# Performance work log

Hardware: AMD Instinct MI355X
Metric: run time of the kernel (lower is better)

The kernel has to match this reference:

```python
import jax, jax.numpy as jnp
import numpy as np
import math

B, S, D, H, NB = 32, 512, 512, 8, 2
DK = D // H
DF = 4 * D
EPS = 1e-8


def layer_norm(x, gamma, beta):
    # Matches torch: unbiased std (ddof=1), divide by (std + eps)
    mean = jnp.mean(x, axis=-1, keepdims=True)
    std = jnp.sqrt(jnp.var(x, axis=-1, keepdims=True, ddof=1))
    return gamma * (x - mean) / (std + EPS) + beta


def block(x, wq, bq, wk, bk, wv, bv, wr, br, ga, ba, wc1, bc1, wc2, bc2, gf, bf):
    # --- attention with ReLU-gated Q/K/V ---
    Q = jax.nn.relu(x @ wq.T + bq)  # [B,S,D]
    K = jax.nn.relu(x @ wk.T + bk)
    V = jax.nn.relu(x @ wv.T + bv)
    # chunk along last dim -> heads; head-major stacking is equivalent to this reshape
    Qh = Q.reshape(B, S, H, DK)
    Kh = K.reshape(B, S, H, DK)
    Vh = V.reshape(B, S, H, DK)
    scores = jnp.einsum('bqhd,bkhd->bhqk', Qh, Kh) / math.sqrt(DK)
    w = jax.nn.softmax(scores, axis=-1)
    out = jnp.einsum('bhqk,bkhd->bqhd', w, Vh).reshape(B, S, D)
    out = out + jax.nn.relu(x @ wr.T + br)
    out = layer_norm(out, ga, ba)
    # --- conv1d (kernel=1) feed-forward ---
    h = jax.nn.relu(out @ wc1.T + bc1)  # [B,S,4D]
    y = h @ wc2.T + bc2                 # [B,S,D]
    y = layer_norm(y + out, gf, bf)
    return y


def setup_inputs() -> dict:
    key = jax.random.key(0)
    ks = jax.random.split(key, 8)
    std = 0.01
    inp = {
        'x': jax.random.normal(ks[0], (B, S, D), jnp.float32),
        'wq': jax.random.normal(ks[1], (NB, D, D), jnp.float32) * std,
        'bq': jnp.zeros((NB, D), jnp.float32),
        'wk': jax.random.normal(ks[2], (NB, D, D), jnp.float32) * std,
        'bk': jnp.zeros((NB, D), jnp.float32),
        'wv': jax.random.normal(ks[3], (NB, D, D), jnp.float32) * std,
        'bv': jnp.zeros((NB, D), jnp.float32),
        'wr': jax.random.normal(ks[4], (NB, D, D), jnp.float32) * std,
        'br': jnp.zeros((NB, D), jnp.float32),
        'g_attn': jnp.ones((NB, D), jnp.float32),
        'b_attn': jnp.zeros((NB, D), jnp.float32),
        'wc1': jax.random.normal(ks[5], (NB, DF, D), jnp.float32) * (1.0 / math.sqrt(D)),
        'bc1': jnp.zeros((NB, DF), jnp.float32),
        'wc2': jax.random.normal(ks[6], (NB, D, DF), jnp.float32) * (1.0 / math.sqrt(DF)),
        'bc2': jnp.zeros((NB, D), jnp.float32),
        'g_ffn': jnp.ones((NB, D), jnp.float32),
        'b_ffn': jnp.zeros((NB, D), jnp.float32),
    }
    return inp


def reference(x, wq, bq, wk, bk, wv, bv, wr, br, g_attn, b_attn,
              wc1, bc1, wc2, bc2, g_ffn, b_ffn):
    enc = x
    for i in range(NB):
        enc = block(enc, wq[i], bq[i], wk[i], bk[i], wv[i], bv[i], wr[i], br[i],
                    g_attn[i], b_attn[i], wc1[i], bc1[i], wc2[i], bc2[i],
                    g_ffn[i], b_ffn[i])
    return enc
```

## Files before the change

### kernel.cpp

```cpp
#include <hip/hip_runtime.h>

typedef unsigned short u16;
typedef __bf16 bf16x8 __attribute__((ext_vector_type(8)));
typedef float f32x4 __attribute__((ext_vector_type(4)));
typedef unsigned short ushort8 __attribute__((ext_vector_type(8)));

__device__ __forceinline__ void gload_lds16(const void* g, void* l) {
  __builtin_amdgcn_global_load_lds(
      (const __attribute__((address_space(1))) void*)g,
      (__attribute__((address_space(3))) void*)l, 16, 0, 0);
}

__device__ __forceinline__ u16 f2bf(float f) {
  unsigned int u = __builtin_bit_cast(unsigned int, f);
  u = (u + 0x7fffu + ((u >> 16) & 1u)) >> 16;
  return (u16)u;
}
__device__ __forceinline__ u16 f2bf_trunc(float f) {
  return (u16)(__builtin_bit_cast(unsigned int, f) >> 16);
}
__device__ __forceinline__ float bf2f(u16 u) {
  unsigned int v = (unsigned int)u << 16;
  return __builtin_bit_cast(float, v);
}

__global__ void castk(const float* __restrict__ in, u16* __restrict__ out, int n,
                      float scale) {
  size_t i = ((size_t)blockIdx.x * 256 + threadIdx.x) * 8;
  if (i >= (size_t)n) return;
  const float4* p = (const float4*)(in + i);
  float4 a = p[0], b = p[1];
  ushort8 o;
  o[0] = f2bf(a.x * scale); o[1] = f2bf(a.y * scale);
  o[2] = f2bf(a.z * scale); o[3] = f2bf(a.w * scale);
  o[4] = f2bf(b.x * scale); o[5] = f2bf(b.y * scale);
  o[6] = f2bf(b.z * scale); o[7] = f2bf(b.w * scale);
  *(ushort8*)(out + i) = o;
}

__global__ void biasg(const float* __restrict__ b0, const float* __restrict__ b1,
                      const float* __restrict__ b2, const float* __restrict__ b3,
                      float* __restrict__ out) {
  int idx = blockIdx.x * 256 + threadIdx.x;
  int i = idx >> 11, j = (idx >> 9) & 3, c = idx & 511;
  const float* src = (j == 0) ? b0 : (j == 1) ? b1 : (j == 2) ? b2 : b3;
  float v = src[i * 512 + c];
  out[idx] = (j == 0) ? v * 0.125f : v;
}

template<int BN, int RELU, int WVT>
__global__ __launch_bounds__(512, 2)
void gemm8(const u16* __restrict__ A, const u16* __restrict__ W,
           const float* __restrict__ bias, u16* __restrict__ C,
           u16* __restrict__ VT, int M, int N, int K)
{
  constexpr int WN = (BN == 256) ? 4 : 2;
  constexpr int WM = 8 / WN;
  constexpr int RM = 256 / WM;
  constexpr int MF = RM / 16;
  constexpr int ASZ = 16384;
  constexpr int BSZ = BN * 64;
  constexpr int ALOADS = 2;
  constexpr int BLOADS = BN / 128;
  constexpr int VC = ALOADS + BLOADS;

  __shared__ u16 lds[(ASZ + BSZ) * 2];
  char* Abase = (char*)lds;
  char* Bbase = (char*)lds + ASZ * 4;

  const int tid = threadIdx.x;
  const int w = tid >> 6, l = tid & 63;
  const int nbn = N / BN;
  const int p = blockIdx.x;
  const int x = p & 7, i0 = p >> 3;
  const int bm = x * 8 + i0 / nbn;
  const int bn = i0 % nbn;
  const int wn = w & (WN - 1);
  const int wm = w / WN;
  const int NK = K >> 5;

  const int srow = l >> 2;
  const int scol = ((l & 3) ^ ((l >> 3) & 3)) << 3;
  const u16* aS[ALOADS];
  const u16* bS[BLOADS];
#pragma unroll
  for (int u = 0; u < ALOADS; ++u)
    aS[u] = A + (size_t)(bm * 256 + (u * 8 + w) * 16 + srow) * K + scol;
#pragma unroll
  for (int u = 0; u < BLOADS; ++u)
    bS[u] = W + (size_t)(bn * BN + (u * 8 + w) * 16 + srow) * K + scol;

  auto stage = [&](int t) {
    const int bsel = t & 3;
#pragma unroll
    for (int u = 0; u < ALOADS; ++u)
      gload_lds16(aS[u] + t * 32, Abase + bsel * ASZ + (u * 8 + w) * 1024);
#pragma unroll
    for (int u = 0; u < BLOADS; ++u)
      gload_lds16(bS[u] + t * 32, Bbase + bsel * BSZ + (u * 8 + w) * 1024);
  };

  f32x4 acc[MF][4] = {};

  stage(0); stage(1); stage(2);

  for (int t = 0; t < NK; ++t) {
    const int rem = NK - 1 - t;
    if (rem >= 2)      asm volatile("s_waitcnt vmcnt(%0)" :: "i"(2 * VC) : "memory");
    else if (rem == 1) asm volatile("s_waitcnt vmcnt(%0)" :: "i"(VC) : "memory");
    else               asm volatile("s_waitcnt vmcnt(0)" ::: "memory");
    __builtin_amdgcn_s_barrier();
    __builtin_amdgcn_sched_barrier(0);
    if (t + 3 < NK) stage(t + 3);

    const char* Ab = Abase + (t & 3) * ASZ;
    const char* Bb = Bbase + (t & 3) * BSZ;
    bf16x8 af[MF], bfv[4];
#pragma unroll
    for (int mi = 0; mi < MF; ++mi) {
      int row = wm * RM + mi * 16 + (l & 15);
      af[mi] = *(const bf16x8*)(Ab + row * 64 + (((l >> 4) ^ ((row >> 1) & 3)) << 4));
    }
#pragma unroll
    for (int ni = 0; ni < 4; ++ni) {
      int row = wn * 64 + ni * 16 + (l & 15);
      bfv[ni] = *(const bf16x8*)(Bb + row * 64 + (((l >> 4) ^ ((row >> 1) & 3)) << 4));
    }
    __builtin_amdgcn_s_setprio(1);
#pragma unroll
    for (int mi = 0; mi < MF; ++mi)
#pragma unroll
      for (int ni = 0; ni < 4; ++ni)
        acc[mi][ni] = __builtin_amdgcn_mfma_f32_16x16x32_bf16(af[mi], bfv[ni], acc[mi][ni], 0, 0, 0);
    __builtin_amdgcn_s_setprio(0);
  }

  __syncthreads();
  char* Ct = (char*)lds;
  const int rowL = wm * RM + ((l >> 4) << 2);
  const int colL = wn * 64 + (l & 15);
  const bool dovt = WVT && (bn == 4 || bn == 5);
  float bv[4];
#pragma unroll
  for (int ni = 0; ni < 4; ++ni) bv[ni] = bias[bn * BN + colL + ni * 16];

  if (!dovt) {
#pragma unroll
    for (int mi = 0; mi < MF; ++mi)
#pragma unroll
      for (int ni = 0; ni < 4; ++ni)
#pragma unroll
        for (int r = 0; r < 4; ++r) {
          float v = acc[mi][ni][r] + bv[ni];
          if (RELU) v = fmaxf(v, 0.f);
          int m = rowL + mi * 16 + r, n = colL + ni * 16;
          *(u16*)(Ct + m * (BN * 2) + ((n * 2) ^ ((m & 7) << 4))) = f2bf(v);
        }
    __syncthreads();
    constexpr int TPR = (BN * 2) / 16;
    constexpr int RPP = 512 / TPR;
#pragma unroll
    for (int pass = 0; pass < 256 / RPP; ++pass) {
      int row = pass * RPP + tid / TPR;
      int c16 = tid % TPR;
      bf16x8 vv = *(const bf16x8*)(Ct + row * (BN * 2) + ((c16 * 16) ^ ((row & 7) << 4)));
      *(bf16x8*)(&C[(size_t)(bm * 256 + row) * N + bn * BN + c16 * 8]) = vv;
    }
  } else {
#pragma unroll
    for (int mi = 0; mi < MF; ++mi)
#pragma unroll
      for (int ni = 0; ni < 4; ++ni)
#pragma unroll
        for (int r = 0; r < 4; ++r) {
          float v = acc[mi][ni][r] + bv[ni];
          if (RELU) v = fmaxf(v, 0.f);
          int m = rowL + mi * 16 + r, d = colL + ni * 16;
          *(u16*)(Ct + d * 512 + ((m * 2) ^ ((d & 7) << 4))) = f2bf(v);
        }
    __syncthreads();
    const int batch = bm >> 1;
#pragma unroll
    for (int pass = 0; pass < 16; ++pass) {
      int dL = pass * 16 + (tid >> 5);
      int m16 = tid & 31;
      bf16x8 vv = *(const bf16x8*)(Ct + dL * 512 + ((m16 * 16) ^ ((dL & 7) << 4)));
      int head = (bn - 4) * 4 + (dL >> 6);
      int vtr = (batch * 8 + head) * 64 + (dL & 63);
      *(bf16x8*)(&VT[(size_t)vtr * 512 + (bm & 1) * 256 + m16 * 8]) = vv;
    }
  }
}

__global__ __launch_bounds__(256, 2)
void attn_kernel(const u16* __restrict__ qkvr, const u16* __restrict__ VT,
                 u16* __restrict__ F)
{
  const int D4 = 2048;
  __shared__ u16 Qs[128 * 64];
  __shared__ u16 Ks[2][64 * 64];
  __shared__ u16 Vs[2][64 * 64];
  __shared__ u16 Ps[128 * 64];

  const int tid = threadIdx.x, w = tid >> 6, l = tid & 63;
  const int bh = blockIdx.x & 255, qt = blockIdx.x >> 8;
  const int b = bh >> 3, h = bh & 7;
  const int lr = l >> 3, lc = ((l & 7) ^ lr) << 3;
  const int l15 = l & 15, lh = l >> 4;

  const u16* qG = qkvr + (size_t)(b * 512 + qt * 128) * D4 + h * 64 + lc;
#pragma unroll
  for (int i = 0; i < 4; ++i) {
    int c = w * 4 + i;
    gload_lds16(qG + (size_t)(c * 8 + lr) * D4, &Qs[c * 512]);
  }

  const u16* kG = qkvr + (size_t)(b * 512) * D4 + 512 + h * 64 + lc;
  const u16* vG = VT + (size_t)(bh * 64) * 512 + lc;

  auto stageKV = [&](int kt) {
    const int bsel = kt & 1;
#pragma unroll
    for (int i = 0; i < 2; ++i) {
      int c = w * 2 + i;
      gload_lds16(kG + (size_t)(kt * 64 + c * 8 + lr) * D4, &Ks[bsel][c * 512]);
      gload_lds16(vG + (size_t)(c * 8 + lr) * 512 + kt * 64, &Vs[bsel][c * 512]);
    }
  };
  stageKV(0);

  f32x4 o_acc[2][4] = {};
  float psum[2][4] = {};

  for (int kt = 0; kt < 8; ++kt) {
    __syncthreads();
    if (kt < 7) stageKV(kt + 1);
    const char* Kb = (const char*)Ks[kt & 1];
    const char* Vb = (const char*)Vs[kt & 1];

    f32x4 sacc[2][4] = {};
#pragma unroll
    for (int kk = 0; kk < 2; ++kk) {
      bf16x8 qa[2];
#pragma unroll
      for (int qq = 0; qq < 2; ++qq) {
        int qrow = w * 32 + qq * 16 + l15;
        qa[qq] = *(const bf16x8*)((const char*)Qs + qrow * 128 +
                  ((kk * 64 + (lh << 4)) ^ ((qrow & 7) << 4)));
      }
#pragma unroll
      for (int ni = 0; ni < 4; ++ni) {
        int krow = ni * 16 + l15;
        bf16x8 kb = *(const bf16x8*)(Kb + krow * 128 +
                    ((kk * 64 + (lh << 4)) ^ ((krow & 7) << 4)));
#pragma unroll
        for (int qq = 0; qq < 2; ++qq)
          sacc[qq][ni] = __builtin_amdgcn_mfma_f32_16x16x32_bf16(qa[qq], kb, sacc[qq][ni], 0, 0, 0);
      }
    }

#pragma unroll
    for (int qq = 0; qq < 2; ++qq)
#pragma unroll
      for (int r = 0; r < 4; ++r) {
        float p0 = __expf(sacc[qq][0][r]);
        float p1 = __expf(sacc[qq][1][r]);
        float p2 = __expf(sacc[qq][2][r]);
        float p3 = __expf(sacc[qq][3][r]);
        psum[qq][r] += (p0 + p1) + (p2 + p3);
        int q = w * 32 + qq * 16 + (lh << 2) + r;
        int sw = (q & 7) << 4;
        int col = l15 * 2;
        char* pb = (char*)Ps + q * 128;
        *(u16*)(pb + ((0  + col) ^ sw)) = f2bf_trunc(p0);
        *(u16*)(pb + ((32 + col) ^ sw)) = f2bf_trunc(p1);
        *(u16*)(pb + ((64 + col) ^ sw)) = f2bf_trunc(p2);
        *(u16*)(pb + ((96 + col) ^ sw)) = f2bf_trunc(p3);
      }

#pragma unroll
    for (int kk = 0; kk < 2; ++kk) {
      bf16x8 pa[2];
#pragma unroll
      for (int qq = 0; qq < 2; ++qq) {
        int qrow = w * 32 + qq * 16 + l15;
        pa[qq] = *(const bf16x8*)((const char*)Ps + qrow * 128 +
                  ((kk * 64 + (lh << 4)) ^ ((qrow & 7) << 4)));
      }
#pragma unroll
      for (int ni = 0; ni < 4; ++ni) {
        int d = ni * 16 + l15;
        bf16x8 vb = *(const bf16x8*)(Vb + d * 128 +
                    ((kk * 64 + (lh << 4)) ^ ((d & 7) << 4)));
#pragma unroll
        for (int qq = 0; qq < 2; ++qq)
          o_acc[qq][ni] = __builtin_amdgcn_mfma_f32_16x16x32_bf16(pa[qq], vb, o_acc[qq][ni], 0, 0, 0);
      }
    }
  }

  float lsum[2][4];
#pragma unroll
  for (int qq = 0; qq < 2; ++qq)
#pragma unroll
    for (int r = 0; r < 4; ++r) {
      float t = psum[qq][r];
#pragma unroll
      for (int m = 1; m < 16; m <<= 1) t += __shfl_xor(t, m);
      lsum[qq][r] = 1.f / t;
    }

#pragma unroll
  for (int qq = 0; qq < 2; ++qq)
#pragma unroll
    for (int ni = 0; ni < 4; ++ni) {
      int d = ni * 16 + l15;
#pragma unroll
      for (int r = 0; r < 4; ++r) {
        float v = o_acc[qq][ni][r] * lsum[qq][r];
        int q = w * 32 + qq * 16 + (lh << 2) + r;
        *(u16*)((char*)Ps + q * 128 + ((d * 2) ^ ((q & 7) << 4))) = f2bf(v);
      }
    }
  __syncthreads();
  const u16* Rbase = qkvr + (size_t)(b * 512 + qt * 128) * D4 + 1536 + h * 64;
  u16* Fbase = F + (size_t)(b * 512 + qt * 128) * 512 + h * 64;
#pragma unroll
  for (int pass = 0; pass < 4; ++pass) {
    int row = pass * 32 + (tid >> 3), c8 = tid & 7;
    ushort8 lv = *(const ushort8*)((char*)Ps + row * 128 + ((c8 * 16) ^ ((row & 7) << 4)));
    ushort8 rv = *(const ushort8*)(Rbase + (size_t)row * D4 + c8 * 8);
    ushort8 o;
#pragma unroll
    for (int j = 0; j < 8; ++j) o[j] = f2bf(bf2f(lv[j]) + bf2f(rv[j]));
    *(ushort8*)(Fbase + (size_t)row * 512 + c8 * 8) = o;
  }
}

template<int HAS_RES, int OUT_F32>
__global__ __launch_bounds__(256)
void ln_bf(const u16* __restrict__ in, const u16* __restrict__ res,
           const float* __restrict__ gamma, const float* __restrict__ beta,
           u16* __restrict__ outb, float* __restrict__ outf)
{
  const int l = threadIdx.x & 63;
  const size_t row = (size_t)blockIdx.x * 4 + (threadIdx.x >> 6);
  ushort8 iv = *(const ushort8*)(in + row * 512 + l * 8);
  float x[8];
#pragma unroll
  for (int j = 0; j < 8; ++j) x[j] = bf2f(iv[j]);
  if (HAS_RES) {
    ushort8 rv = *(const ushort8*)(res + row * 512 + l * 8);
#pragma unroll
    for (int j = 0; j < 8; ++j) x[j] += bf2f(rv[j]);
  }
  float s = 0.f, ss = 0.f;
#pragma unroll
  for (int j = 0; j < 8; ++j) { s += x[j]; ss += x[j] * x[j]; }
#pragma unroll
  for (int m = 1; m < 64; m <<= 1) { s += __shfl_xor(s, m); ss += __shfl_xor(ss, m); }
  float mean = s * (1.f / 512.f);
  float var = fmaxf((ss - 512.f * mean * mean) * (1.f / 511.f), 0.f);
  float inv = 1.f / (sqrtf(var) + 1e-8f);
  const float4* g4 = (const float4*)gamma;
  const float4* b4 = (const float4*)beta;
  float4 g0 = g4[l * 2], g1 = g4[l * 2 + 1];
  float4 b0 = b4[l * 2], b1 = b4[l * 2 + 1];
  float gg[8] = {g0.x, g0.y, g0.z, g0.w, g1.x, g1.y, g1.z, g1.w};
  float bb[8] = {b0.x, b0.y, b0.z, b0.w, b1.x, b1.y, b1.z, b1.w};
  float y[8];
#pragma unroll
  for (int j = 0; j < 8; ++j) y[j] = gg[j] * (x[j] - mean) * inv + bb[j];
  ushort8 o;
#pragma unroll
  for (int j = 0; j < 8; ++j) o[j] = f2bf(y[j]);
  *(ushort8*)(outb + row * 512 + l * 8) = o;
  if (OUT_F32) {
    float4* o4 = (float4*)(outf + row * 512);
    o4[l * 2]     = make_float4(y[0], y[1], y[2], y[3]);
    o4[l * 2 + 1] = make_float4(y[4], y[5], y[6], y[7]);
  }
}

extern "C" void kernel_launch(void* const* d_in, const int* in_sizes, int n_in,
                              void* d_out, int out_size, void* d_ws, size_t ws_size,
                              hipStream_t stream)
{
  const int B = 32, S = 512, D = 512, NB = 2, DF = 2048;
  const int M = B * S;

  const float* x   = (const float*)d_in[0];
  const float* wsrc[4] = {(const float*)d_in[1], (const float*)d_in[3],
                          (const float*)d_in[5], (const float*)d_in[7]};
  const float* ga  = (const float*)d_in[9];
  const float* ba  = (const float*)d_in[10];
  const float* wc1 = (const float*)d_in[11];
  const float* bc1 = (const float*)d_in[12];
  const float* wc2 = (const float*)d_in[13];
  const float* bc2 = (const float*)d_in[14];
  const float* gf  = (const float*)d_in[15];
  const float* bfp = (const float*)d_in[16];

  char* ws = (char*)d_ws;
  u16*   curb = (u16*)(ws + 0);
  u16*   qkvr = (u16*)(ws + 16777216);
  u16*   F    = (u16*)(ws + 83886080);
  u16*   Hg   = (u16*)(ws + 100663296);
  u16*   VT   = (u16*)(ws + 117440512);
  u16*   w4b  = (u16*)(ws + 134217728);
  u16*   wc1b = (u16*)(ws + 138412032);
  u16*   wc2b = (u16*)(ws + 142606336);
  float* b4   = (float*)(ws + 146800640);
  u16*   Ih   = qkvr;
  u16*   Y    = F;

  castk<<<M * D / 2048, 256, 0, stream>>>(x, curb, M * D, 1.0f);
  for (int i = 0; i < NB; ++i)
    for (int j = 0; j < 4; ++j)
      castk<<<128, 256, 0, stream>>>(wsrc[j] + (size_t)i * 262144,
                                     w4b + (size_t)i * 1048576 + j * 262144, 262144,
                                     (j == 0) ? 0.125f : 1.0f);
  biasg<<<16, 256, 0, stream>>>((const float*)d_in[2], (const float*)d_in[4],
                                (const float*)d_in[6], (const float*)d_in[8], b4);
  castk<<<NB * DF * D / 2048, 256, 0, stream>>>(wc1, wc1b, NB * DF * D, 1.0f);
  castk<<<NB * DF * D / 2048, 256, 0, stream>>>(wc2, wc2b, NB * DF * D, 1.0f);

  for (int i = 0; i < NB; ++i) {
    const size_t wfo = (size_t)i * DF * D;
    gemm8<256, 1, 1><<<512, 512, 0, stream>>>(curb, w4b + (size_t)i * 1048576,
                                              b4 + i * 2048, qkvr, VT, M, 2048, 512);
    attn_kernel<<<4 * 256, 256, 0, stream>>>(qkvr, VT, F);
    ln_bf<0, 0><<<M / 4, 256, 0, stream>>>(F, nullptr, ga + i * D, ba + i * D, Hg, nullptr);
    gemm8<256, 1, 0><<<512, 512, 0, stream>>>(Hg, wc1b + wfo, bc1 + i * DF,
                                              Ih, nullptr, M, 2048, 512);
    gemm8<128, 0, 0><<<256, 512, 0, stream>>>(Ih, wc2b + wfo, bc2 + i * D,
                                              Y, nullptr, M, 512, 2048);
    if (i == NB - 1)
      ln_bf<1, 1><<<M / 4, 256, 0, stream>>>(Y, Hg, gf + i * D, bfp + i * D,
                                             curb, (float*)d_out);
    else
      ln_bf<1, 0><<<M / 4, 256, 0, stream>>>(Y, Hg, gf + i * D, bfp + i * D,
                                             curb, nullptr);
  }
}
```

Before: 395.0 us.

## Restructure bf16 GEMM into 8-wave ping-pong pipeline with 64-wide K tiles

Replaces the GEMM main loop's 4-deep ring of 32-wide K stages with double-buffered 64-wide K tiles split into M and N halves. Each iteration runs four MFMA quadrants separated by barriers, and loads for the next tile are issued between them. Every wave now covers a 128-row M slice, and the layout switches to a 128-byte-row LDS swizzle. The goal is better overlap of global-to-LDS loads with MFMA work and fewer barriers per unit of K. In exchange it uses more accumulator and fragment registers plus extra intra-iteration barriers, which could lower occupancy under the 2-blocks-per-CU launch bound.

```diff
diff --git a/kernel.cpp b/kernel.cpp
--- a/kernel.cpp
+++ b/kernel.cpp
@@ -50,105 +50,113 @@
 
 template<int BN, int RELU, int WVT>
 __global__ __launch_bounds__(512, 2)
-void gemm8(const u16* __restrict__ A, const u16* __restrict__ W,
-           const float* __restrict__ bias, u16* __restrict__ C,
-           u16* __restrict__ VT, int M, int N, int K)
+void gemm256(const u16* __restrict__ A, const u16* __restrict__ W,
+             const float* __restrict__ bias, u16* __restrict__ C,
+             u16* __restrict__ VT, int M, int N, int K)
 {
-  constexpr int WN = (BN == 256) ? 4 : 2;
-  constexpr int WM = 8 / WN;
-  constexpr int RM = 256 / WM;
-  constexpr int MF = RM / 16;
-  constexpr int ASZ = 16384;
-  constexpr int BSZ = BN * 64;
-  constexpr int ALOADS = 2;
-  constexpr int BLOADS = BN / 128;
-  constexpr int VC = ALOADS + BLOADS;
-
-  __shared__ u16 lds[(ASZ + BSZ) * 2];
-  char* Abase = (char*)lds;
-  char* Bbase = (char*)lds + ASZ * 4;
-
-  const int tid = threadIdx.x;
-  const int w = tid >> 6, l = tid & 63;
+  constexpr int CN   = BN / 4;
+  constexpr int NF   = CN / 32;
+  constexpr int NTOT = CN / 16;
+  constexpr int ATSZ = 256 * 128;
+  constexpr int BTSZ = BN * 128;
+  constexpr int BLH  = BN / 128;
+
+  __shared__ char lds[2 * (ATSZ + BTSZ)];
+  char* ABase = lds;
+  char* BBase = lds + 2 * ATSZ;
+
+  const int tid = threadIdx.x, w = tid >> 6, l = tid & 63;
+  const int l15 = l & 15, lh = l >> 4;
   const int nbn = N / BN;
   const int p = blockIdx.x;
-  const int x = p & 7, i0 = p >> 3;
-  const int bm = x * 8 + i0 / nbn;
-  const int bn = i0 % nbn;
-  const int wn = w & (WN - 1);
-  const int wm = w / WN;
-  const int NK = K >> 5;
-
-  const int srow = l >> 2;
-  const int scol = ((l & 3) ^ ((l >> 3) & 3)) << 3;
-  const u16* aS[ALOADS];
-  const u16* bS[BLOADS];
-#pragma unroll
-  for (int u = 0; u < ALOADS; ++u)
-    aS[u] = A + (size_t)(bm * 256 + (u * 8 + w) * 16 + srow) * K + scol;
-#pragma unroll
-  for (int u = 0; u < BLOADS; ++u)
-    bS[u] = W + (size_t)(bn * BN + (u * 8 + w) * 16 + srow) * K + scol;
-
-  auto stage = [&](int t) {
-    const int bsel = t & 3;
-#pragma unroll
-    for (int u = 0; u < ALOADS; ++u)
-      gload_lds16(aS[u] + t * 32, Abase + bsel * ASZ + (u * 8 + w) * 1024);
-#pragma unroll
-    for (int u = 0; u < BLOADS; ++u)
-      gload_lds16(bS[u] + t * 32, Bbase + bsel * BSZ + (u * 8 + w) * 1024);
-  };
-
-  f32x4 acc[MF][4] = {};
-
-  stage(0); stage(1); stage(2);
-
-  for (int t = 0; t < NK; ++t) {
-    const int rem = NK - 1 - t;
-    if (rem >= 2)      asm volatile("s_waitcnt vmcnt(%0)" :: "i"(2 * VC) : "memory");
-    else if (rem == 1) asm volatile("s_waitcnt vmcnt(%0)" :: "i"(VC) : "memory");
-    else               asm volatile("s_waitcnt vmcnt(0)" ::: "memory");
+  const int bm = (p & 7) * 8 + (p >> 3) / nbn;
+  const int bn = (p >> 3) % nbn;
+  const int wm = w >> 2, wn = w & 3;
+  const int NT = K >> 6;
+
+  const int srow = l >> 3;
+  const int scol = ((l & 7) ^ srow) << 3;
+  const u16* aG = A + (size_t)(bm * 256 + srow) * K + scol;
+  const u16* bG = W + (size_t)(bn * BN + srow) * K + scol;
+
+#define STAGE_A(T, H)                                                          \
+  { _Pragma("unroll") for (int i = 0; i < 2; ++i)                              \
+      gload_lds16(aG + (size_t)((H) * 128 + (w * 2 + i) * 8) * K + (T) * 64,   \
+                  ABase + ((T) & 1) * ATSZ + (H) * 16384 + (w * 2 + i) * 1024); }
+#define STAGE_B(T, H)                                                          \
+  { _Pragma("unroll") for (int i = 0; i < BLH; ++i)                            \
+      gload_lds16(bG + (size_t)((H) * (BN / 2) + (w * BLH + i) * 8) * K + (T) * 64, \
+                  BBase + ((T) & 1) * BTSZ + (H) * (BTSZ / 2) + (w * BLH + i) * 1024); }
+#define READ_A(MH)                                                             \
+  { _Pragma("unroll") for (int kk = 0; kk < 2; ++kk)                           \
+    _Pragma("unroll") for (int mf = 0; mf < 4; ++mf) {                         \
+      int row = wm * 128 + (MH) * 64 + mf * 16 + l15;                          \
+      a[kk][mf] = *(const bf16x8*)(Ab + row * 128 +                            \
+                   ((kk * 64 + lh * 16) ^ ((l15 & 7) << 4)));                  \
+    } }
+#define READ_B(NH)                                                             \
+  { _Pragma("unroll") for (int kk = 0; kk < 2; ++kk)                           \
+    _Pragma("unroll") for (int nf = 0; nf < NF; ++nf) {                        \
+      int row = wn * CN + (NH) * (CN / 2) + nf * 16 + l15;                     \
+      bb[NH][kk][nf] = *(const bf16x8*)(Bb + row * 128 +                       \
+                        ((kk * 64 + lh * 16) ^ ((l15 & 7) << 4)));             \
+    } }
+#define DO_MFMA(MH, NH)                                                        \
+  { __builtin_amdgcn_s_setprio(1);                                             \
+    _Pragma("unroll") for (int mf = 0; mf < 4; ++mf)                           \
+    _Pragma("unroll") for (int nf = 0; nf < NF; ++nf)                          \
+    _Pragma("unroll") for (int kk = 0; kk < 2; ++kk)                           \
+      acc[(MH) * 4 + mf][(NH) * NF + nf] =                                     \
+        __builtin_amdgcn_mfma_f32_16x16x32_bf16(a[kk][mf], bb[NH][kk][nf],     \
+            acc[(MH) * 4 + mf][(NH) * NF + nf], 0, 0, 0);                      \
+    __builtin_amdgcn_s_setprio(0); }
+
+  STAGE_A(0, 0); STAGE_A(0, 1); STAGE_B(0, 0); STAGE_B(0, 1); STAGE_B(1, 0);
+
+  f32x4 acc[8][NTOT] = {};
+  bf16x8 a[2][4], bb[2][2][NF];
+
+  for (int u = 0; u < NT; ++u) {
+    const char* Ab = ABase + (u & 1) * ATSZ;
+    const char* Bb = BBase + (u & 1) * BTSZ;
+    const bool more = (u + 1 < NT);
+    if (more) asm volatile("s_waitcnt vmcnt(%0)" :: "i"(BLH) : "memory");
+    else      asm volatile("s_waitcnt vmcnt(0)" ::: "memory");
     __builtin_amdgcn_s_barrier();
-    __builtin_amdgcn_sched_barrier(0);
-    if (t + 3 < NK) stage(t + 3);
-
-    const char* Ab = Abase + (t & 3) * ASZ;
-    const char* Bb = Bbase + (t & 3) * BSZ;
-    bf16x8 af[MF], bfv[4];
-#pragma unroll
-    for (int mi = 0; mi < MF; ++mi) {
-      int row = wm * RM + mi * 16 + (l & 15);
-      af[mi] = *(const bf16x8*)(Ab + row * 64 + (((l >> 4) ^ ((row >> 1) & 3)) << 4));
-    }
-#pragma unroll
-    for (int ni = 0; ni < 4; ++ni) {
-      int row = wn * 64 + ni * 16 + (l & 15);
-      bfv[ni] = *(const bf16x8*)(Bb + row * 64 + (((l >> 4) ^ ((row >> 1) & 3)) << 4));
-    }
-    __builtin_amdgcn_s_setprio(1);
-#pragma unroll
-    for (int mi = 0; mi < MF; ++mi)
-#pragma unroll
-      for (int ni = 0; ni < 4; ++ni)
-        acc[mi][ni] = __builtin_amdgcn_mfma_f32_16x16x32_bf16(af[mi], bfv[ni], acc[mi][ni], 0, 0, 0);
-    __builtin_amdgcn_s_setprio(0);
-  }
+    READ_A(0); READ_B(0);
+    if (more) { STAGE_A(u + 1, 0); STAGE_B(u + 1, 1); }
+    DO_MFMA(0, 0);
+    __builtin_amdgcn_s_barrier();
+    READ_B(1);
+    if (more) { STAGE_A(u + 1, 1); }
+    DO_MFMA(0, 1);
+    __builtin_amdgcn_s_barrier();
+    READ_A(1);
+    DO_MFMA(1, 0);
+    __builtin_amdgcn_s_barrier();
+    if (u + 2 < NT) { STAGE_B(u + 2, 0); }
+    DO_MFMA(1, 1);
+  }
+#undef STAGE_A
+#undef STAGE_B
+#undef READ_A
+#undef READ_B
+#undef DO_MFMA
 
   __syncthreads();
   char* Ct = (char*)lds;
-  const int rowL = wm * RM + ((l >> 4) << 2);
-  const int colL = wn * 64 + (l & 15);
+  const int rowL = wm * 128 + (lh << 2);
+  const int colL = wn * CN + l15;
   const bool dovt = WVT && (bn == 4 || bn == 5);
-  float bv[4];
-#pragma unroll
-  for (int ni = 0; ni < 4; ++ni) bv[ni] = bias[bn * BN + colL + ni * 16];
+  float bv[NTOT];
+#pragma unroll
+  for (int ni = 0; ni < NTOT; ++ni) bv[ni] = bias[bn * BN + colL + ni * 16];
 
   if (!dovt) {
 #pragma unroll
-    for (int mi = 0; mi < MF; ++mi)
-#pragma unroll
-      for (int ni = 0; ni < 4; ++ni)
+    for (int mi = 0; mi < 8; ++mi)
+#pragma unroll
+      for (int ni = 0; ni < NTOT; ++ni)
 #pragma unroll
         for (int r = 0; r < 4; ++r) {
           float v = acc[mi][ni][r] + bv[ni];
@@ -168,9 +176,9 @@
     }
   } else {
 #pragma unroll
-    for (int mi = 0; mi < MF; ++mi)
-#pragma unroll
-      for (int ni = 0; ni < 4; ++ni)
+    for (int mi = 0; mi < 8; ++mi)
+#pragma unroll
+      for (int ni = 0; ni < NTOT; ++ni)
 #pragma unroll
         for (int r = 0; r < 4; ++r) {
           float v = acc[mi][ni][r] + bv[ni];
@@ -427,14 +435,14 @@
 
   for (int i = 0; i < NB; ++i) {
     const size_t wfo = (size_t)i * DF * D;
-    gemm8<256, 1, 1><<<512, 512, 0, stream>>>(curb, w4b + (size_t)i * 1048576,
-                                              b4 + i * 2048, qkvr, VT, M, 2048, 512);
+    gemm256<256, 1, 1><<<512, 512, 0, stream>>>(curb, w4b + (size_t)i * 1048576,
+                                                b4 + i * 2048, qkvr, VT, M, 2048, 512);
     attn_kernel<<<4 * 256, 256, 0, stream>>>(qkvr, VT, F);
     ln_bf<0, 0><<<M / 4, 256, 0, stream>>>(F, nullptr, ga + i * D, ba + i * D, Hg, nullptr);
-    gemm8<256, 1, 0><<<512, 512, 0, stream>>>(Hg, wc1b + wfo, bc1 + i * DF,
-                                              Ih, nullptr, M, 2048, 512);
-    gemm8<128, 0, 0><<<256, 512, 0, stream>>>(Ih, wc2b + wfo, bc2 + i * D,
-                                              Y, nullptr, M, 512, 2048);
+    gemm256<256, 1, 0><<<512, 512, 0, stream>>>(Hg, wc1b + wfo, bc1 + i * DF,
+                                                Ih, nullptr, M, 2048, 512);
+    gemm256<128, 0, 0><<<256, 512, 0, stream>>>(Ih, wc2b + wfo, bc2 + i * D,
+                                                Y, nullptr, M, 512, 2048);
     if (i == NB - 1)
       ln_bf<1, 1><<<M / 4, 256, 0, stream>>>(Y, Hg, gf + i * D, bfp + i * D,
                                              curb, (float*)d_out);
```

After: 382.8 us. -3.1%, faster.

## Shrink GEMM M-tile to 128 rows with double buffering and higher occupancy

Applied to the files above, without the earlier changes.

Replaces the 256-row GEMM tile with a 128-row tile. Pipelining changes from a 4-stage to a 2-stage LDS ring that waits on all loads with vmcnt(0), and launch bounds rise to 4 blocks per CU. The grid doubles, giving more blocks per CU and better load balance across the MI355X's CUs, and LDS use per block shrinks. In exchange each block reuses its operands less (more global/L2 traffic per FLOP), prefetch depth is shallower, and the register budget per thread tightens.

```diff
diff --git a/kernel.cpp b/kernel.cpp
--- a/kernel.cpp
+++ b/kernel.cpp
@@ -49,145 +49,133 @@
 }
 
 template<int BN, int RELU, int WVT>
-__global__ __launch_bounds__(512, 2)
-void gemm8(const u16* __restrict__ A, const u16* __restrict__ W,
-           const float* __restrict__ bias, u16* __restrict__ C,
-           u16* __restrict__ VT, int M, int N, int K)
+__global__ __launch_bounds__(512, 4)
+void gemm128(const u16* __restrict__ A, const u16* __restrict__ W,
+             const float* __restrict__ bias, u16* __restrict__ C,
+             u16* __restrict__ VT, int M, int N, int K)
 {
-  constexpr int WN = (BN == 256) ? 4 : 2;
-  constexpr int WM = 8 / WN;
-  constexpr int RM = 256 / WM;
-  constexpr int MF = RM / 16;
-  constexpr int ASZ = 16384;
-  constexpr int BSZ = BN * 64;
-  constexpr int ALOADS = 2;
-  constexpr int BLOADS = BN / 128;
-  constexpr int VC = ALOADS + BLOADS;
-
-  __shared__ u16 lds[(ASZ + BSZ) * 2];
-  char* Abase = (char*)lds;
-  char* Bbase = (char*)lds + ASZ * 4;
-
-  const int tid = threadIdx.x;
-  const int w = tid >> 6, l = tid & 63;
+  constexpr int CN   = BN / 4;
+  constexpr int NF   = CN / 16;
+  constexpr int ATSZ = 128 * 64;
+  constexpr int BTSZ = BN * 64;
+  constexpr int BLB  = BN / 128;
+  constexpr int PSZ  = 2 * (ATSZ + BTSZ);
+  constexpr int ESZ  = 128 * BN * 2;
+  constexpr int LSZ  = (PSZ > ESZ) ? PSZ : ESZ;
+
+  __shared__ char lds[LSZ];
+  char* ABase = lds;
+  char* BBase = lds + 2 * ATSZ;
+
+  const int tid = threadIdx.x, w = tid >> 6, l = tid & 63;
+  const int l15 = l & 15, lh = l >> 4;
   const int nbn = N / BN;
   const int p = blockIdx.x;
-  const int x = p & 7, i0 = p >> 3;
-  const int bm = x * 8 + i0 / nbn;
-  const int bn = i0 % nbn;
-  const int wn = w & (WN - 1);
-  const int wm = w / WN;
-  const int NK = K >> 5;
+  const int bm = (p & 7) * 16 + (p >> 3) / nbn;
+  const int bn = (p >> 3) % nbn;
+  const int wm = w >> 2, wn = w & 3;
+  const int NT = K >> 5;
 
   const int srow = l >> 2;
   const int scol = ((l & 3) ^ ((l >> 3) & 3)) << 3;
-  const u16* aS[ALOADS];
-  const u16* bS[BLOADS];
-#pragma unroll
-  for (int u = 0; u < ALOADS; ++u)
-    aS[u] = A + (size_t)(bm * 256 + (u * 8 + w) * 16 + srow) * K + scol;
-#pragma unroll
-  for (int u = 0; u < BLOADS; ++u)
-    bS[u] = W + (size_t)(bn * BN + (u * 8 + w) * 16 + srow) * K + scol;
+  const u16* aS = A + (size_t)(bm * 128 + w * 16 + srow) * K + scol;
+  const u16* bS[BLB];
+#pragma unroll
+  for (int j = 0; j < BLB; ++j)
+    bS[j] = W + (size_t)(bn * BN + (w * BLB + j) * 16 + srow) * K + scol;
 
   auto stage = [&](int t) {
-    const int bsel = t & 3;
-#pragma unroll
-    for (int u = 0; u < ALOADS; ++u)
-      gload_lds16(aS[u] + t * 32, Abase + bsel * ASZ + (u * 8 + w) * 1024);
-#pragma unroll
-    for (int u = 0; u < BLOADS; ++u)
-      gload_lds16(bS[u] + t * 32, Bbase + bsel * BSZ + (u * 8 + w) * 1024);
+    gload_lds16(aS + t * 32, ABase + (t & 1) * ATSZ + w * 1024);
+#pragma unroll
+    for (int j = 0; j < BLB; ++j)
+      gload_lds16(bS[j] + t * 32, BBase + (t & 1) * BTSZ + (w * BLB + j) * 1024);
   };
 
-  f32x4 acc[MF][4] = {};
-
-  stage(0); stage(1); stage(2);
-
-  for (int t = 0; t < NK; ++t) {
-    const int rem = NK - 1 - t;
-    if (rem >= 2)      asm volatile("s_waitcnt vmcnt(%0)" :: "i"(2 * VC) : "memory");
-    else if (rem == 1) asm volatile("s_waitcnt vmcnt(%0)" :: "i"(VC) : "memory");
-    else               asm volatile("s_waitcnt vmcnt(0)" ::: "memory");
+  f32x4 acc[4][NF] = {};
+  const int sw = ((l15 >> 1) & 3) << 4;
+
+  stage(0);
+  for (int u = 0; u < NT; ++u) {
+    asm volatile("s_waitcnt vmcnt(0)" ::: "memory");
     __builtin_amdgcn_s_barrier();
     __builtin_amdgcn_sched_barrier(0);
-    if (t + 3 < NK) stage(t + 3);
-
-    const char* Ab = Abase + (t & 3) * ASZ;
-    const char* Bb = Bbase + (t & 3) * BSZ;
-    bf16x8 af[MF], bfv[4];
-#pragma unroll
-    for (int mi = 0; mi < MF; ++mi) {
-      int row = wm * RM + mi * 16 + (l & 15);
-      af[mi] = *(const bf16x8*)(Ab + row * 64 + (((l >> 4) ^ ((row >> 1) & 3)) << 4));
-    }
-#pragma unroll
-    for (int ni = 0; ni < 4; ++ni) {
-      int row = wn * 64 + ni * 16 + (l & 15);
-      bfv[ni] = *(const bf16x8*)(Bb + row * 64 + (((l >> 4) ^ ((row >> 1) & 3)) << 4));
+    if (u + 1 < NT) stage(u + 1);
+
+    const char* Ab = ABase + (u & 1) * ATSZ;
+    const char* Bb = BBase + (u & 1) * BTSZ;
+    bf16x8 a[4], b[NF];
+#pragma unroll
+    for (int mf = 0; mf < 4; ++mf) {
+      int row = wm * 64 + mf * 16 + l15;
+      a[mf] = *(const bf16x8*)(Ab + row * 64 + ((lh << 4) ^ sw));
+    }
+#pragma unroll
+    for (int nf = 0; nf < NF; ++nf) {
+      int row = wn * CN + nf * 16 + l15;
+      b[nf] = *(const bf16x8*)(Bb + row * 64 + ((lh << 4) ^ sw));
     }
     __builtin_amdgcn_s_setprio(1);
 #pragma unroll
-    for (int mi = 0; mi < MF; ++mi)
-#pragma unroll
-      for (int ni = 0; ni < 4; ++ni)
-        acc[mi][ni] = __builtin_amdgcn_mfma_f32_16x16x32_bf16(af[mi], bfv[ni], acc[mi][ni], 0, 0, 0);
+    for (int mf = 0; mf < 4; ++mf)
+#pragma unroll
+      for (int nf = 0; nf < NF; ++nf)
+        acc[mf][nf] = __builtin_amdgcn_mfma_f32_16x16x32_bf16(a[mf], b[nf], acc[mf][nf], 0, 0, 0);
     __builtin_amdgcn_s_setprio(0);
   }
 
   __syncthreads();
   char* Ct = (char*)lds;
-  const int rowL = wm * RM + ((l >> 4) << 2);
-  const int colL = wn * 64 + (l & 15);
+  const int rowL = wm * 64 + (lh << 2);
+  const int colL = wn * CN + l15;
   const bool dovt = WVT && (bn == 4 || bn == 5);
-  float bv[4];
-#pragma unroll
-  for (int ni = 0; ni < 4; ++ni) bv[ni] = bias[bn * BN + colL + ni * 16];
+  float bv[NF];
+#pragma unroll
+  for (int nf = 0; nf < NF; ++nf) bv[nf] = bias[bn * BN + colL + nf * 16];
 
   if (!dovt) {
 #pragma unroll
-    for (int mi = 0; mi < MF; ++mi)
-#pragma unroll
-      for (int ni = 0; ni < 4; ++ni)
+    for (int mf = 0; mf < 4; ++mf)
+#pragma unroll
+      for (int nf = 0; nf < NF; ++nf)
 #pragma unroll
         for (int r = 0; r < 4; ++r) {
-          float v = acc[mi][ni][r] + bv[ni];
+          float v = acc[mf][nf][r] + bv[nf];
           if (RELU) v = fmaxf(v, 0.f);
-          int m = rowL + mi * 16 + r, n = colL + ni * 16;
+          int m = rowL + mf * 16 + r, n = colL + nf * 16;
           *(u16*)(Ct + m * (BN * 2) + ((n * 2) ^ ((m & 7) << 4))) = f2bf(v);
         }
     __syncthreads();
     constexpr int TPR = (BN * 2) / 16;
     constexpr int RPP = 512 / TPR;
 #pragma unroll
-    for (int pass = 0; pass < 256 / RPP; ++pass) {
+    for (int pass = 0; pass < 128 / RPP; ++pass) {
       int row = pass * RPP + tid / TPR;
       int c16 = tid % TPR;
       bf16x8 vv = *(const bf16x8*)(Ct + row * (BN * 2) + ((c16 * 16) ^ ((row & 7) << 4)));
-      *(bf16x8*)(&C[(size_t)(bm * 256 + row) * N + bn * BN + c16 * 8]) = vv;
+      *(bf16x8*)(&C[(size_t)(bm * 128 + row) * N + bn * BN + c16 * 8]) = vv;
     }
   } else {
 #pragma unroll
-    for (int mi = 0; mi < MF; ++mi)
-#pragma unroll
-      for (int ni = 0; ni < 4; ++ni)
+    for (int mf = 0; mf < 4; ++mf)
+#pragma unroll
+      for (int nf = 0; nf < NF; ++nf)
 #pragma unroll
         for (int r = 0; r < 4; ++r) {
-          float v = acc[mi][ni][r] + bv[ni];
+          float v = acc[mf][nf][r] + bv[nf];
           if (RELU) v = fmaxf(v, 0.f);
-          int m = rowL + mi * 16 + r, d = colL + ni * 16;
-          *(u16*)(Ct + d * 512 + ((m * 2) ^ ((d & 7) << 4))) = f2bf(v);
+          int m = rowL + mf * 16 + r, d = colL + nf * 16;
+          *(u16*)(Ct + d * 256 + ((m * 2) ^ ((d & 7) << 4))) = f2bf(v);
         }
     __syncthreads();
-    const int batch = bm >> 1;
-#pragma unroll
-    for (int pass = 0; pass < 16; ++pass) {
-      int dL = pass * 16 + (tid >> 5);
-      int m16 = tid & 31;
-      bf16x8 vv = *(const bf16x8*)(Ct + dL * 512 + ((m16 * 16) ^ ((dL & 7) << 4)));
+    const int batch = bm >> 2;
+#pragma unroll
+    for (int pass = 0; pass < 8; ++pass) {
+      int dL = pass * 32 + (tid >> 4);
+      int m16 = tid & 15;
+      bf16x8 vv = *(const bf16x8*)(Ct + dL * 256 + ((m16 * 16) ^ ((dL & 7) << 4)));
       int head = (bn - 4) * 4 + (dL >> 6);
       int vtr = (batch * 8 + head) * 64 + (dL & 63);
-      *(bf16x8*)(&VT[(size_t)vtr * 512 + (bm & 1) * 256 + m16 * 8]) = vv;
+      *(bf16x8*)(&VT[(size_t)vtr * 512 + (bm & 3) * 128 + m16 * 8]) = vv;
     }
   }
 }
@@ -427,14 +415,14 @@
 
   for (int i = 0; i < NB; ++i) {
     const size_t wfo = (size_t)i * DF * D;
-    gemm8<256, 1, 1><<<512, 512, 0, stream>>>(curb, w4b + (size_t)i * 1048576,
-                                              b4 + i * 2048, qkvr, VT, M, 2048, 512);
+    gemm128<256, 1, 1><<<1024, 512, 0, stream>>>(curb, w4b + (size_t)i * 1048576,
+                                                 b4 + i * 2048, qkvr, VT, M, 2048, 512);
     attn_kernel<<<4 * 256, 256, 0, stream>>>(qkvr, VT, F);
     ln_bf<0, 0><<<M / 4, 256, 0, stream>>>(F, nullptr, ga + i * D, ba + i * D, Hg, nullptr);
-    gemm8<256, 1, 0><<<512, 512, 0, stream>>>(Hg, wc1b + wfo, bc1 + i * DF,
-                                              Ih, nullptr, M, 2048, 512);
-    gemm8<128, 0, 0><<<256, 512, 0, stream>>>(Ih, wc2b + wfo, bc2 + i * D,
-                                              Y, nullptr, M, 512, 2048);
+    gemm128<256, 1, 0><<<1024, 512, 0, stream>>>(Hg, wc1b + wfo, bc1 + i * DF,
+                                                 Ih, nullptr, M, 2048, 512);
+    gemm128<128, 0, 0><<<512, 512, 0, stream>>>(Ih, wc2b + wfo, bc2 + i * D,
+                                                Y, nullptr, M, 512, 2048);
     if (i == NB - 1)
       ln_bf<1, 1><<<M / 4, 256, 0, stream>>>(Y, Hg, gf + i * D, bfp + i * D,
                                              curb, (float*)d_out);
```

Result: no change. 387.5 us (-1.9%).
